# Optimization experiments

Hardware: AMD Instinct MI355X
Metric: run time of the kernel (lower is better)

Reference implementation:

```python
import jax, jax.numpy as jnp
import numpy as np

B, S, D_IN, D_H, D_OUT, NB = 4, 4096, 1024, 1024, 1024, 8
BD = D_H // NB  # block size of the block-diagonal gate projections
R_MIN, R_MAX, EPS = 0.9, 0.999, 1e-8


def setup_inputs() -> dict:
    key = jax.random.key(0)
    ks = jax.random.split(key, 8)
    x = jax.random.normal(ks[0], (B, S, D_IN), dtype=jnp.float32)
    h0 = jnp.zeros((B, D_H), dtype=jnp.float32)
    # input projection Dense(d_hidden)
    W_in = jax.random.normal(ks[1], (D_IN, D_H), dtype=jnp.float32) / np.sqrt(D_IN)
    b_in = jnp.zeros((D_H,), dtype=jnp.float32)
    # two BlockDiagonalLinear gate projections (n_blocks blocks of [BD, BD])
    Wgx = jax.random.normal(ks[2], (NB, BD, BD), dtype=jnp.float32) / np.sqrt(BD)
    bgx = jnp.zeros((D_H,), dtype=jnp.float32)
    Wga = jax.random.normal(ks[3], (NB, BD, BD), dtype=jnp.float32) / np.sqrt(BD)
    bga = jnp.zeros((D_H,), dtype=jnp.float32)
    # stable_init_real: softplus(param) == -log(r) with r ~ U[r_min, r_max] in magnitude
    u = jax.random.uniform(ks[4], (D_H,), dtype=jnp.float32)
    a_real = 0.5 * jnp.log(u * (R_MAX**2 - R_MIN**2) + R_MIN**2 + EPS)
    a_real_param = jnp.log(jnp.exp(-a_real) - 1.0)
    # output projection Dense(d_out)
    W_out = jax.random.normal(ks[5], (D_H, D_OUT), dtype=jnp.float32) / np.sqrt(D_H)
    b_out = jnp.zeros((D_OUT,), dtype=jnp.float32)
    return dict(x=x, h0=h0, W_in=W_in, b_in=b_in, Wgx=Wgx, bgx=bgx,
                Wga=Wga, bga=bga, a_real_param=a_real_param,
                W_out=W_out, b_out=b_out)


def _block_diag_linear(x, W, b):
    # x: [B,S,D_H] -> split into NB blocks of BD, per-block matmul
    xb = x.reshape(x.shape[0], x.shape[1], NB, BD)
    y = jnp.einsum('bsni,nio->bsno', xb, W)
    return y.reshape(x.shape[0], x.shape[1], D_H) + b


def reference(x, h0, W_in, b_in, Wgx, bgx, Wga, bga, a_real_param, W_out, b_out):
    # input projection
    x = x @ W_in + b_in  # [B,S,D_H]
    # input-dependent gates (sigmoid of block-diagonal projections)
    gate_x = jax.nn.sigmoid(_block_diag_linear(x, Wgx, bgx))
    gate_a = jax.nn.sigmoid(_block_diag_linear(x, Wga, bga))
    # real-only RG-LRU recurrence coefficient: a = exp(-8 * gate_a * softplus(c))
    log_a = -8.0 * gate_a * jax.nn.softplus(a_real_param)  # [B,S,D_H], <= 0
    a = jnp.exp(log_a)
    # gated input with sqrt(1 - a^2) normalization (sqrt_bound_derivative fwd == sqrt)
    gx = gate_x * x * jnp.sqrt(1.0 - jnp.exp(2.0 * log_a))
    # fold initial state into the first step: h_1 = a_1 * h0 + gx_1
    gx = gx.at[:, 0].add(a[:, 0] * h0)
    # linear scan h_t = a_t * h_{t-1} + gx_t via associative scan over seq axis
    def combine(c1, c2):
        a1, x1 = c1
        a2, x2 = c2
        return (a2 * a1, a2 * x1 + x2)
    _, h = jax.lax.associative_scan(combine, (a, gx), axis=1)  # [B,S,D_H]
    out = h @ W_out + b_out  # [B,S,D_OUT]
    return out, h[:, -1]
```

## Files before the change

### kernel.cpp

```cpp
#include <hip/hip_runtime.h>

#define B_SZ 4
#define SEQ 4096
#define DIN 1024
#define DH 1024
#define DOUT 1024
#define NBLK 8
#define MTOK (B_SZ * SEQ)
#define CHUNK 64
#define NCHUNK (SEQ / CHUNK)

typedef _Float16 half8 __attribute__((ext_vector_type(8)));
typedef _Float16 half4v __attribute__((ext_vector_type(4)));
typedef float f32x4 __attribute__((ext_vector_type(4)));

union HPack { unsigned int u; _Float16 h[2]; };

__device__ __forceinline__ void gl_lds16(const void* g, void* l) {
  __builtin_amdgcn_global_load_lds((__attribute__((address_space(1))) void*)g,
                                   (__attribute__((address_space(3))) void*)l,
                                   16, 0, 0);
}

__device__ __forceinline__ int swz_h(int r, int c) {
  return (((r << 8) | (c << 1)) ^ ((r & 7) << 4)) >> 1;
}

__global__ __launch_bounds__(256)
void prep_kernel(const float* __restrict__ x, _Float16* __restrict__ x_h,
                 const float* __restrict__ Win, const float* __restrict__ Wout,
                 const float* __restrict__ Wgx, const float* __restrict__ Wga,
                 _Float16* __restrict__ WinT, _Float16* __restrict__ WoutT,
                 _Float16* __restrict__ WgxT, _Float16* __restrict__ WgaT) {
  __shared__ float tile[64][65];
  if (blockIdx.x < 16384) {
    const int gid = blockIdx.x * 256 + threadIdx.x;
    const float4 v = ((const float4*)x)[gid];
    half4v h;
    h[0] = (_Float16)v.x; h[1] = (_Float16)v.y; h[2] = (_Float16)v.z; h[3] = (_Float16)v.w;
    ((half4v*)x_h)[gid] = h;
    return;
  }
  int t = blockIdx.x - 16384;
  const float* src; _Float16* dst; int C; size_t bo = 0;
  if (t < 256)      { src = Win;  dst = WinT;  C = 1024; }
  else if (t < 512) { src = Wout; dst = WoutT; C = 1024; t -= 256; }
  else if (t < 544) { int u = t - 512; src = Wgx; dst = WgxT; C = 128;
                      bo = (size_t)(u >> 2) * (128 * 128); t = u & 3; }
  else              { int u = t - 544; src = Wga; dst = WgaT; C = 128;
                      bo = (size_t)(u >> 2) * (128 * 128); t = u & 3; }
  const int nbx = C >> 6;
  const int r0 = (t / nbx) * 64, c0 = (t % nbx) * 64;
  const int tr = threadIdx.x >> 6, tc = threadIdx.x & 63;
#pragma unroll
  for (int i = 0; i < 64; i += 4)
    tile[tr + i][tc] = src[bo + (size_t)(r0 + tr + i) * C + c0 + tc];
  __syncthreads();
#pragma unroll
  for (int i = 0; i < 64; i += 4) {
    const int cc = i + tr;
    dst[bo + (size_t)(c0 + cc) * C + r0 + tc] = (_Float16)tile[tc][cc];
  }
}

template <int OUT_F32>
__global__ __launch_bounds__(256, 4)
void gemm_bt(const _Float16* __restrict__ A, const _Float16* __restrict__ Bt,
             const float* __restrict__ bias, void* __restrict__ C,
             int M, int N, int K) {
  __shared__ __align__(16) _Float16 As[128 * 64];
  __shared__ __align__(16) _Float16 Bs[128 * 64];
  const int tid = threadIdx.x;
  const int wave = tid >> 6, lane = tid & 63;
  const int m0 = blockIdx.x * 128, n0 = blockIdx.y * 128;
  const int wm = (wave >> 1) * 64, wn = (wave & 1) * 64;
  const int row = lane & 15, quad = lane >> 4;
  const int srow = lane >> 3, scol = (lane & 7) * 8;

  f32x4 acc[4][4] = {};
#pragma unroll 1
  for (int kt = 0; kt < K; kt += 64) {
#pragma unroll
    for (int ci = 0; ci < 4; ci++) {
      const int c = wave * 4 + ci;
      gl_lds16(A  + (size_t)(m0 + c * 8 + srow) * K + kt + scol, As + c * 512);
      gl_lds16(Bt + (size_t)(n0 + c * 8 + srow) * K + kt + scol, Bs + c * 512);
    }
    __syncthreads();
#pragma unroll
    for (int kk = 0; kk < 64; kk += 32) {
      half8 af[4], bf[4];
#pragma unroll
      for (int i = 0; i < 4; i++)
        af[i] = *(const half8*)&As[(wm + i * 16 + row) * 64 + kk + quad * 8];
#pragma unroll
      for (int i = 0; i < 4; i++)
        bf[i] = *(const half8*)&Bs[(wn + i * 16 + row) * 64 + kk + quad * 8];
#pragma unroll
      for (int i = 0; i < 4; i++)
#pragma unroll
        for (int j = 0; j < 4; j++)
          acc[i][j] = __builtin_amdgcn_mfma_f32_16x16x32_f16(af[i], bf[j], acc[i][j], 0, 0, 0);
    }
    __syncthreads();
  }
  float bv[4];
#pragma unroll
  for (int j = 0; j < 4; j++) bv[j] = bias[n0 + wn + j * 16 + row];
#pragma unroll
  for (int i = 0; i < 4; i++) {
#pragma unroll
    for (int r = 0; r < 4; r++) {
      const int m = m0 + wm + i * 16 + quad * 4 + r;
      const size_t base = (size_t)m * N + n0 + wn + row;
#pragma unroll
      for (int j = 0; j < 4; j++) {
        const float v = acc[i][j][r] + bv[j];
        if (OUT_F32) ((float*)C)[base + j * 16] = v;
        else         ((_Float16*)C)[base + j * 16] = (_Float16)v;
      }
    }
  }
}

__global__ __launch_bounds__(256, 4)
void gemm1_gates(const _Float16* __restrict__ A, const _Float16* __restrict__ Bt,
                 const float* __restrict__ bias,
                 const _Float16* __restrict__ WxT, const _Float16* __restrict__ WaT,
                 const float* __restrict__ bgx, const float* __restrict__ bga,
                 const float* __restrict__ arp,
                 unsigned int* __restrict__ ag,
                 float* __restrict__ cA, float* __restrict__ cH) {
  __shared__ __align__(16) _Float16 smem[128 * 128];
  _Float16* const As = smem;
  _Float16* const Bs = smem + 128 * 64;
  const int tid = threadIdx.x;
  const int wave = tid >> 6, lane = tid & 63;
  const int m0 = blockIdx.x * 128, nb = blockIdx.y, n0 = nb * 128;
  const int wm = (wave >> 1) * 64, wn = (wave & 1) * 64;
  const int row = lane & 15, quad = lane >> 4;
  const int srow = lane >> 3, scol = (lane & 7) * 8;

  f32x4 acc[4][4] = {};
#pragma unroll 1
  for (int kt = 0; kt < DIN; kt += 64) {
#pragma unroll
    for (int ci = 0; ci < 4; ci++) {
      const int c = wave * 4 + ci;
      gl_lds16(A  + (size_t)(m0 + c * 8 + srow) * DIN + kt + scol, As + c * 512);
      gl_lds16(Bt + (size_t)(n0 + c * 8 + srow) * DIN + kt + scol, Bs + c * 512);
    }
    __syncthreads();
#pragma unroll
    for (int kk = 0; kk < 64; kk += 32) {
      half8 af[4], bf[4];
#pragma unroll
      for (int i = 0; i < 4; i++)
        af[i] = *(const half8*)&As[(wm + i * 16 + row) * 64 + kk + quad * 8];
#pragma unroll
      for (int i = 0; i < 4; i++)
        bf[i] = *(const half8*)&Bs[(wn + i * 16 + row) * 64 + kk + quad * 8];
#pragma unroll
      for (int i = 0; i < 4; i++)
#pragma unroll
        for (int j = 0; j < 4; j++)
          acc[i][j] = __builtin_amdgcn_mfma_f32_16x16x32_f16(af[i], bf[j], acc[i][j], 0, 0, 0);
    }
    __syncthreads();
  }

  {
    float bv[4];
#pragma unroll
    for (int j = 0; j < 4; j++) bv[j] = bias[n0 + wn + j * 16 + row];
#pragma unroll
    for (int i = 0; i < 4; i++)
#pragma unroll
      for (int r = 0; r < 4; r++) {
        const int tl = wm + i * 16 + quad * 4 + r;
#pragma unroll
        for (int j = 0; j < 4; j++)
          smem[swz_h(tl, wn + j * 16 + row)] = (_Float16)(acc[i][j][r] + bv[j]);
      }
  }
  __syncthreads();

  const _Float16* const WxB = WxT + (size_t)nb * (128 * 128);
  const _Float16* const WaB = WaT + (size_t)nb * (128 * 128);
  const int b_idx = (m0 + wm) >> 12;
  const int c_idx = ((m0 + wm) & (SEQ - 1)) >> 6;
  const int cbase = c_idx * (B_SZ * DH) + b_idx * DH + n0 + wn + row;
  const size_t agbase = ((size_t)(blockIdx.x * NBLK + nb) * 4 + wave) * 4096;

#pragma unroll 1
  for (int jp = 0; jp < 2; jp++) {
    f32x4 accx[4][2] = {}, acca[4][2] = {};
#pragma unroll
    for (int kk = 0; kk < 128; kk += 32) {
      half8 af[4];
#pragma unroll
      for (int i = 0; i < 4; i++)
        af[i] = *(const half8*)&smem[swz_h(wm + i * 16 + row, kk + quad * 8)];
#pragma unroll
      for (int jj = 0; jj < 2; jj++) {
        const size_t wo = (size_t)(wn + (jp * 2 + jj) * 16 + row) * 128 + kk + quad * 8;
        const half8 bx = *(const half8*)&WxB[wo];
        const half8 ba = *(const half8*)&WaB[wo];
#pragma unroll
        for (int i = 0; i < 4; i++) {
          accx[i][jj] = __builtin_amdgcn_mfma_f32_16x16x32_f16(af[i], bx, accx[i][jj], 0, 0, 0);
          acca[i][jj] = __builtin_amdgcn_mfma_f32_16x16x32_f16(af[i], ba, acca[i][jj], 0, 0, 0);
        }
      }
    }
    float bxv[2], bav[2], cd[2];
#pragma unroll
    for (int jj = 0; jj < 2; jj++) {
      const int d = n0 + wn + (jp * 2 + jj) * 16 + row;
      bxv[jj] = bgx[d]; bav[jj] = bga[d];
      cd[jj] = log1pf(expf(arp[d]));
    }
    float Arun[2] = {1.f, 1.f}, Hrun[2] = {0.f, 0.f};
#pragma unroll
    for (int i = 0; i < 4; i++) {
      float Aseg[2] = {1.f, 1.f}, Hseg[2] = {0.f, 0.f};
#pragma unroll
      for (int r = 0; r < 4; r++) {
        const int tl = wm + i * 16 + quad * 4 + r;
#pragma unroll
        for (int jj = 0; jj < 2; jj++) {
          const float px = accx[i][jj][r] + bxv[jj];
          const float pa = acca[i][jj][r] + bav[jj];
          const float sx = 1.f / (1.f + __expf(-px));
          const float sa = 1.f / (1.f + __expf(-pa));
          const float a = __expf(-8.f * sa * cd[jj]);
          const float n2 = fmaxf(1.f - a * a, 0.f);
          const float xv = (float)smem[swz_h(tl, wn + (jp * 2 + jj) * 16 + row)];
          HPack pk;
          pk.h[0] = (_Float16)a;
          pk.h[1] = (_Float16)(sx * xv * sqrtf(n2));
          ag[agbase + (size_t)(((i * 4 + r) * 4) + jp * 2 + jj) * 64 + lane] = pk.u;
          const float ar = (float)pk.h[0], gr = (float)pk.h[1];
          Aseg[jj] *= ar;
          Hseg[jj] = fmaf(ar, Hseg[jj], gr);
        }
      }
#pragma unroll
      for (int jj = 0; jj < 2; jj++) {
        float A1 = Aseg[jj], H1 = Hseg[jj];
        float A2 = __shfl_down(A1, 16, 64), H2 = __shfl_down(H1, 16, 64);
        H1 = fmaf(A2, H1, H2); A1 *= A2;
        A2 = __shfl_down(A1, 32, 64); H2 = __shfl_down(H1, 32, 64);
        H1 = fmaf(A2, H1, H2); A1 *= A2;
        Hrun[jj] = fmaf(A1, Hrun[jj], H1);
        Arun[jj] *= A1;
      }
    }
    if (lane < 16) {
#pragma unroll
      for (int jj = 0; jj < 2; jj++) {
        cA[cbase + (jp * 2 + jj) * 16] = Arun[jj];
        cH[cbase + (jp * 2 + jj) * 16] = Hrun[jj];
      }
    }
  }
}

__global__ __launch_bounds__(256)
void scan_p2(const float* __restrict__ cA, const float* __restrict__ cH,
             const float* __restrict__ h0, float* __restrict__ cin,
             float* __restrict__ hlast) {
  const int wave = threadIdx.x >> 6, lane = threadIdx.x & 63;
  const int g = blockIdx.x * 4 + wave;
  float A = cA[(size_t)lane * (B_SZ * DH) + g], H = cH[(size_t)lane * (B_SZ * DH) + g];
#pragma unroll
  for (int d = 1; d < 64; d <<= 1) {
    const float Ap = __shfl_up(A, d, 64), Hp = __shfl_up(H, d, 64);
    if (lane >= d) { H = fmaf(A, Hp, H); A *= Ap; }
  }
  const float h0g = h0[g];
  if (lane == 63) hlast[g] = fmaf(A, h0g, H);
  float Ae = __shfl_up(A, 1, 64), He = __shfl_up(H, 1, 64);
  if (lane == 0) { Ae = 1.f; He = 0.f; }
  cin[(size_t)lane * (B_SZ * DH) + g] = fmaf(Ae, h0g, He);
}

__global__ __launch_bounds__(256)
void scan_p3(const unsigned int* __restrict__ ag,
             const float* __restrict__ cin, _Float16* __restrict__ h) {
  const int gtid = blockIdx.x * 256 + threadIdx.x;
  const int d = gtid & (DH - 1);
  const int bc = gtid >> 10;
  const int b = bc >> 6, c = bc & (NCHUNK - 1);
  const int mblk = b * 32 + (c >> 1), wmb = c & 1;
  const int nb = d >> 7, wnb = (d >> 6) & 1, j = (d >> 4) & 3, row = d & 15;
  const size_t agb = ((size_t)(mblk * NBLK + nb) * 4 + wmb * 2 + wnb) * 4096
                   + j * 64 + row;
  const size_t hbase = ((size_t)(b * SEQ + c * CHUNK)) * DH + d;
  float carry = cin[c * (B_SZ * DH) + b * DH + d];
#pragma unroll 8
  for (int t = 0; t < CHUNK; t++) {
    HPack pk;
    pk.u = ag[agb + (size_t)(((t >> 4) * 4 + (t & 3)) * 4) * 64 + ((t >> 2) & 3) * 16];
    const float av = (float)pk.h[0];
    const float gv = (float)pk.h[1];
    carry = fmaf(av, carry, gv);
    h[hbase + (size_t)t * DH] = (_Float16)carry;
  }
}

extern "C" void kernel_launch(void* const* d_in, const int* in_sizes, int n_in,
                              void* d_out, int out_size, void* d_ws, size_t ws_size,
                              hipStream_t stream) {
  const float* x     = (const float*)d_in[0];
  const float* h0    = (const float*)d_in[1];
  const float* W_in  = (const float*)d_in[2];
  const float* b_in  = (const float*)d_in[3];
  const float* Wgx   = (const float*)d_in[4];
  const float* bgx   = (const float*)d_in[5];
  const float* Wga   = (const float*)d_in[6];
  const float* bga   = (const float*)d_in[7];
  const float* arp   = (const float*)d_in[8];
  const float* W_out = (const float*)d_in[9];
  const float* b_out = (const float*)d_in[10];
  float* out = (float*)d_out;
  float* hlast = out + (size_t)MTOK * DOUT;

  char* p = (char*)d_ws;
  auto take = [&](size_t bytes) { char* r = p; p += (bytes + 255) & ~(size_t)255; return r; };
  _Float16* x_h   = (_Float16*)take((size_t)MTOK * DIN * 2);
  unsigned int* ag = (unsigned int*)take((size_t)MTOK * DH * 4);
  _Float16* WinT  = (_Float16*)take((size_t)DIN * DH * 2);
  _Float16* WoutT = (_Float16*)take((size_t)DH * DOUT * 2);
  _Float16* WgxT  = (_Float16*)take((size_t)NBLK * 128 * 128 * 2);
  _Float16* WgaT  = (_Float16*)take((size_t)NBLK * 128 * 128 * 2);
  float* cA   = (float*)take((size_t)NCHUNK * B_SZ * DH * 4);
  float* cH   = (float*)take((size_t)NCHUNK * B_SZ * DH * 4);
  float* cin  = (float*)take((size_t)NCHUNK * B_SZ * DH * 4);
  _Float16* h_buf = x_h;

  prep_kernel<<<16384 + 576, 256, 0, stream>>>(x, x_h, W_in, W_out, Wgx, Wga,
                                               WinT, WoutT, WgxT, WgaT);
  gemm1_gates<<<dim3(MTOK / 128, NBLK), 256, 0, stream>>>(
      x_h, WinT, b_in, WgxT, WgaT, bgx, bga, arp, ag, cA, cH);
  scan_p2<<<(B_SZ * DH) / 4, 256, 0, stream>>>(cA, cH, h0, cin, hlast);
  scan_p3<<<(B_SZ * NCHUNK * DH) / 256, 256, 0, stream>>>(ag, cin, h_buf);
  gemm_bt<1><<<dim3(MTOK / 128, DOUT / 128), 256, 0, stream>>>(h_buf, WoutT, b_out, out, MTOK, DOUT, DH);
}
```

Measured before the change: 300.4 us.

## Double-buffer GEMM K-loop with swizzled LDS and N-major block order

Rewrites the main K loops of both GEMM kernels as a two-stage pipeline over 32-wide K slices. The next slice is fetched with global_load_lds into the other LDS buffer while MFMAs run on the current one, using explicit vmcnt waits and raw barriers in place of full __syncthreads. It also XOR-swizzles the LDS layout to reduce bank conflicts, and swaps the grid axes so that consecutive blocks share the same A rows, which should improve L2 reuse. The risks are hand-written waitcnt correctness and more barriers per unit of K work.

```diff
diff --git a/kernel.cpp b/kernel.cpp
--- a/kernel.cpp
+++ b/kernel.cpp
@@ -20,6 +20,12 @@
   __builtin_amdgcn_global_load_lds((__attribute__((address_space(1))) void*)g,
                                    (__attribute__((address_space(3))) void*)l,
                                    16, 0, 0);
+}
+
+__device__ __forceinline__ void bar_fence() {
+  asm volatile("" ::: "memory");
+  __builtin_amdgcn_s_barrier();
+  asm volatile("" ::: "memory");
 }
 
 __device__ __forceinline__ int swz_h(int r, int c) {
@@ -68,42 +74,58 @@
 void gemm_bt(const _Float16* __restrict__ A, const _Float16* __restrict__ Bt,
              const float* __restrict__ bias, void* __restrict__ C,
              int M, int N, int K) {
-  __shared__ __align__(16) _Float16 As[128 * 64];
-  __shared__ __align__(16) _Float16 Bs[128 * 64];
+  __shared__ __align__(16) _Float16 smem[16384];
   const int tid = threadIdx.x;
   const int wave = tid >> 6, lane = tid & 63;
-  const int m0 = blockIdx.x * 128, n0 = blockIdx.y * 128;
+  const int n0 = blockIdx.x * 128, m0 = blockIdx.y * 128;
   const int wm = (wave >> 1) * 64, wn = (wave & 1) * 64;
   const int row = lane & 15, quad = lane >> 4;
-  const int srow = lane >> 3, scol = (lane & 7) * 8;
+  const int srow = lane >> 2;
+  const int ssl  = ((lane & 3) ^ (srow & 3)) * 8;
+  const int sslot = (quad ^ (row & 3)) * 8;
+
+  auto stage = [&](int kt, int buf) {
+#pragma unroll
+    for (int ci = 0; ci < 2; ci++) {
+      const int c = wave * 2 + ci;
+      gl_lds16(A  + (size_t)(m0 + c * 16 + srow) * K + kt + ssl, smem + buf + c * 512);
+      gl_lds16(Bt + (size_t)(n0 + c * 16 + srow) * K + kt + ssl, smem + 8192 + buf + c * 512);
+    }
+  };
 
   f32x4 acc[4][4] = {};
+  stage(0, 0);
+  stage(32, 4096);
+  asm volatile("s_waitcnt vmcnt(4)" ::: "memory");
+  bar_fence();
+
+  const int nt = K >> 5;
+  int co = 0;
 #pragma unroll 1
-  for (int kt = 0; kt < K; kt += 64) {
-#pragma unroll
-    for (int ci = 0; ci < 4; ci++) {
-      const int c = wave * 4 + ci;
-      gl_lds16(A  + (size_t)(m0 + c * 8 + srow) * K + kt + scol, As + c * 512);
-      gl_lds16(Bt + (size_t)(n0 + c * 8 + srow) * K + kt + scol, Bs + c * 512);
-    }
-    __syncthreads();
-#pragma unroll
-    for (int kk = 0; kk < 64; kk += 32) {
-      half8 af[4], bf[4];
-#pragma unroll
-      for (int i = 0; i < 4; i++)
-        af[i] = *(const half8*)&As[(wm + i * 16 + row) * 64 + kk + quad * 8];
-#pragma unroll
-      for (int i = 0; i < 4; i++)
-        bf[i] = *(const half8*)&Bs[(wn + i * 16 + row) * 64 + kk + quad * 8];
-#pragma unroll
-      for (int i = 0; i < 4; i++)
-#pragma unroll
-        for (int j = 0; j < 4; j++)
-          acc[i][j] = __builtin_amdgcn_mfma_f32_16x16x32_f16(af[i], bf[j], acc[i][j], 0, 0, 0);
-    }
-    __syncthreads();
-  }
+  for (int t = 0; t < nt; ++t) {
+    half8 af[4], bf[4];
+#pragma unroll
+    for (int i = 0; i < 4; i++)
+      af[i] = *(const half8*)&smem[co + (wm + i * 16 + row) * 32 + sslot];
+#pragma unroll
+    for (int j = 0; j < 4; j++)
+      bf[j] = *(const half8*)&smem[8192 + co + (wn + j * 16 + row) * 32 + sslot];
+#pragma unroll
+    for (int i = 0; i < 4; i++)
+#pragma unroll
+      for (int j = 0; j < 4; j++)
+        acc[i][j] = __builtin_amdgcn_mfma_f32_16x16x32_f16(af[i], bf[j], acc[i][j], 0, 0, 0);
+    bar_fence();
+    if (t + 2 < nt) {
+      stage((t + 2) * 32, co);
+      asm volatile("s_waitcnt vmcnt(4)" ::: "memory");
+    } else {
+      asm volatile("s_waitcnt vmcnt(0)" ::: "memory");
+    }
+    bar_fence();
+    co ^= 4096;
+  }
+
   float bv[4];
 #pragma unroll
   for (int j = 0; j < 4; j++) bv[j] = bias[n0 + wn + j * 16 + row];
@@ -131,42 +153,56 @@
                  const float* __restrict__ arp,
                  unsigned int* __restrict__ ag,
                  float* __restrict__ cA, float* __restrict__ cH) {
-  __shared__ __align__(16) _Float16 smem[128 * 128];
-  _Float16* const As = smem;
-  _Float16* const Bs = smem + 128 * 64;
+  __shared__ __align__(16) _Float16 smem[16384];
   const int tid = threadIdx.x;
   const int wave = tid >> 6, lane = tid & 63;
-  const int m0 = blockIdx.x * 128, nb = blockIdx.y, n0 = nb * 128;
+  const int nb = blockIdx.x, n0 = nb * 128, m0 = blockIdx.y * 128;
   const int wm = (wave >> 1) * 64, wn = (wave & 1) * 64;
   const int row = lane & 15, quad = lane >> 4;
-  const int srow = lane >> 3, scol = (lane & 7) * 8;
+  const int srow = lane >> 2;
+  const int ssl  = ((lane & 3) ^ (srow & 3)) * 8;
+  const int sslot = (quad ^ (row & 3)) * 8;
+
+  auto stage = [&](int kt, int buf) {
+#pragma unroll
+    for (int ci = 0; ci < 2; ci++) {
+      const int c = wave * 2 + ci;
+      gl_lds16(A  + (size_t)(m0 + c * 16 + srow) * DIN + kt + ssl, smem + buf + c * 512);
+      gl_lds16(Bt + (size_t)(n0 + c * 16 + srow) * DIN + kt + ssl, smem + 8192 + buf + c * 512);
+    }
+  };
 
   f32x4 acc[4][4] = {};
+  stage(0, 0);
+  stage(32, 4096);
+  asm volatile("s_waitcnt vmcnt(4)" ::: "memory");
+  bar_fence();
+
+  const int nt = DIN >> 5;
+  int co = 0;
 #pragma unroll 1
-  for (int kt = 0; kt < DIN; kt += 64) {
-#pragma unroll
-    for (int ci = 0; ci < 4; ci++) {
-      const int c = wave * 4 + ci;
-      gl_lds16(A  + (size_t)(m0 + c * 8 + srow) * DIN + kt + scol, As + c * 512);
-      gl_lds16(Bt + (size_t)(n0 + c * 8 + srow) * DIN + kt + scol, Bs + c * 512);
-    }
-    __syncthreads();
-#pragma unroll
-    for (int kk = 0; kk < 64; kk += 32) {
-      half8 af[4], bf[4];
-#pragma unroll
-      for (int i = 0; i < 4; i++)
-        af[i] = *(const half8*)&As[(wm + i * 16 + row) * 64 + kk + quad * 8];
-#pragma unroll
-      for (int i = 0; i < 4; i++)
-        bf[i] = *(const half8*)&Bs[(wn + i * 16 + row) * 64 + kk + quad * 8];
-#pragma unroll
-      for (int i = 0; i < 4; i++)
-#pragma unroll
-        for (int j = 0; j < 4; j++)
-          acc[i][j] = __builtin_amdgcn_mfma_f32_16x16x32_f16(af[i], bf[j], acc[i][j], 0, 0, 0);
-    }
-    __syncthreads();
+  for (int t = 0; t < nt; ++t) {
+    half8 af[4], bf[4];
+#pragma unroll
+    for (int i = 0; i < 4; i++)
+      af[i] = *(const half8*)&smem[co + (wm + i * 16 + row) * 32 + sslot];
+#pragma unroll
+    for (int j = 0; j < 4; j++)
+      bf[j] = *(const half8*)&smem[8192 + co + (wn + j * 16 + row) * 32 + sslot];
+#pragma unroll
+    for (int i = 0; i < 4; i++)
+#pragma unroll
+      for (int j = 0; j < 4; j++)
+        acc[i][j] = __builtin_amdgcn_mfma_f32_16x16x32_f16(af[i], bf[j], acc[i][j], 0, 0, 0);
+    bar_fence();
+    if (t + 2 < nt) {
+      stage((t + 2) * 32, co);
+      asm volatile("s_waitcnt vmcnt(4)" ::: "memory");
+    } else {
+      asm volatile("s_waitcnt vmcnt(0)" ::: "memory");
+    }
+    bar_fence();
+    co ^= 4096;
   }
 
   {
@@ -190,7 +226,7 @@
   const int b_idx = (m0 + wm) >> 12;
   const int c_idx = ((m0 + wm) & (SEQ - 1)) >> 6;
   const int cbase = c_idx * (B_SZ * DH) + b_idx * DH + n0 + wn + row;
-  const size_t agbase = ((size_t)(blockIdx.x * NBLK + nb) * 4 + wave) * 4096;
+  const size_t agbase = ((size_t)(blockIdx.y * NBLK + nb) * 4 + wave) * 4096;
 
 #pragma unroll 1
   for (int jp = 0; jp < 2; jp++) {
@@ -341,9 +377,9 @@
 
   prep_kernel<<<16384 + 576, 256, 0, stream>>>(x, x_h, W_in, W_out, Wgx, Wga,
                                                WinT, WoutT, WgxT, WgaT);
-  gemm1_gates<<<dim3(MTOK / 128, NBLK), 256, 0, stream>>>(
+  gemm1_gates<<<dim3(NBLK, MTOK / 128), 256, 0, stream>>>(
       x_h, WinT, b_in, WgxT, WgaT, bgx, bga, arp, ag, cA, cH);
   scan_p2<<<(B_SZ * DH) / 4, 256, 0, stream>>>(cA, cH, h0, cin, hlast);
   scan_p3<<<(B_SZ * NCHUNK * DH) / 256, 256, 0, stream>>>(ag, cin, h_buf);
-  gemm_bt<1><<<dim3(MTOK / 128, DOUT / 128), 256, 0, stream>>>(h_buf, WoutT, b_out, out, MTOK, DOUT, DH);
-}
+  gemm_bt<1><<<dim3(DOUT / 128, MTOK / 128), 256, 0, stream>>>(h_buf, WoutT, b_out, out, MTOK, DOUT, DH);
+}
```

Result: slower. 313.0 us (+4.2%).
